# Performance work log

Measured on AMD Instinct MI355X. Metric: run time of the kernel, lower is better.

The kernel has to match this reference:

```python
import jax, jax.numpy as jnp
import numpy as np

NEG_BIG = -9e15
ALPHA = 0.2  # LeakyReLU negative slope
B, N, F_IN, F_OUT = 8, 2048, 128, 128


def setup_inputs() -> dict:
    key = jax.random.key(0)
    k1, k2, k3, k4 = jax.random.split(key, 4)
    inp = jax.random.normal(k1, (B, N, F_IN), dtype=jnp.float32)
    adj = jax.random.randint(k2, (B, N, N), 0, 2, dtype=jnp.int32)
    W = 0.02 * jax.random.normal(k3, (F_OUT, F_IN), dtype=jnp.float32)  # nn.Linear weight [out,in]
    a = 0.02 * jax.random.normal(k4, (1, 2 * F_OUT), dtype=jnp.float32)  # attention vector [1, 2F]
    return {"input": inp, "adj": adj, "W": W, "a": a}


def reference(input, adj, W, a):
    # h = input @ W^T : [B, N, F_OUT]
    h = jnp.einsum("bnf,of->bno", input, W)
    f_out = h.shape[-1]
    # Decompose a . [h_i || h_j] = (h_i . a1) + (h_j . a2) -- same math as the
    # explicit repeat_interleave/repeat/cat, without the O(N^2 * 2F) tensor.
    a1 = a[0, :f_out]
    a2 = a[0, f_out:]
    s1 = h @ a1  # [B, N] score for source node i
    s2 = h @ a2  # [B, N] score for target node j
    e = jax.nn.leaky_relu(s1[:, :, None] + s2[:, None, :], negative_slope=ALPHA)  # [B,N,N]
    masked = jnp.where(adj > 0, e, NEG_BIG)
    attention = jax.nn.softmax(masked, axis=-1)
    # dropout p=0.0 (eval) -> identity
    h_prime = jnp.einsum("bnm,bmo->bno", attention, h)
    return h_prime
```

## Files before the change

kernel.cpp:

```cpp
#include <hip/hip_runtime.h>
#include <stdint.h>


#define B_ 8
#define N_ 2048
#define FD 128
#define ALPHA_ 0.2f
#define TJ 64
#define NCHL 16
#define CHUNK_U4 1024

typedef __attribute__((ext_vector_type(8))) short short8;
typedef __attribute__((ext_vector_type(4))) float f32x4;

#define HCHUNK(o, jc) ((((o) * 16) + ((jc) ^ ((o) & 15))) * 8)
#define HC64(o, jc) ((o) * 8 + ((jc) ^ ((o) & 7)))

__device__ __forceinline__ float bf2f(unsigned short u) {
    union { uint32_t i; float f; } v; v.i = ((uint32_t)u) << 16; return v.f;
}
__device__ __forceinline__ unsigned short f2bf(float f) {
    union { float f; uint32_t i; } v; v.f = f;
    uint32_t x = v.i;
    uint32_t r = (x + 0x7fffu + ((x >> 16) & 1u)) >> 16;
    return (unsigned short)r;
}

__device__ __forceinline__ void gl2lds16(const uint4* g, uint4* l) {
    __builtin_amdgcn_global_load_lds(
        (const __attribute__((address_space(1))) uint32_t*)g,
        (__attribute__((address_space(3))) uint32_t*)l, 16, 0, 0);
}

__global__ __launch_bounds__(256) void gat_h(
    const float* __restrict__ x,
    const float* __restrict__ W,
    const float* __restrict__ a,
    unsigned short* __restrict__ hT,
    float* __restrict__ s1o, float* __restrict__ s2o)
{
    __shared__ __align__(16) unsigned short Wlds[FD * FD];
    __shared__ __align__(16) uint4 xs[64][32];

    const int bid = blockIdx.x;
    const int tid = threadIdx.x;
    const int w = tid >> 6;
    const int lane = tid & 63;
    const int m = lane & 15;
    const int quad = lane >> 4;

#pragma unroll
    for (int it = 0; it < 8; it++) {
        int cid = it * 256 + tid;
        int o = cid >> 4, kc = cid & 15;
        const float* wp = W + (size_t)o * FD + kc * 8;
        float4 w0 = *(const float4*)wp;
        float4 w1 = *(const float4*)(wp + 4);
        uint4 pk;
        pk.x = (uint32_t)f2bf(w0.x) | ((uint32_t)f2bf(w0.y) << 16);
        pk.y = (uint32_t)f2bf(w0.z) | ((uint32_t)f2bf(w0.w) << 16);
        pk.z = (uint32_t)f2bf(w1.x) | ((uint32_t)f2bf(w1.y) << 16);
        pk.w = (uint32_t)f2bf(w1.z) | ((uint32_t)f2bf(w1.w) << 16);
        *(uint4*)&Wlds[HCHUNK(o, kc)] = pk;
    }
#pragma unroll
    for (int it = 0; it < 8; it++) {
        int idx = it * 256 + tid;
        int row = idx >> 5, c = idx & 31;
        uint4 v = *(const uint4*)(x + (size_t)bid * 8192 + (size_t)idx * 4);
        xs[row][c ^ (row & 31)] = v;
    }
    __syncthreads();

    f32x4 acc[8];
#pragma unroll
    for (int ot = 0; ot < 8; ot++) acc[ot] = (f32x4){0.f, 0.f, 0.f, 0.f};

    const int xrow = w * 16 + m;
#pragma unroll
    for (int ks = 0; ks < 4; ks++) {
        const int c0 = ks * 8 + quad * 2;
        union { uint4 u[2]; float f[8]; } xv;
        xv.u[0] = xs[xrow][c0 ^ (xrow & 31)];
        xv.u[1] = xs[xrow][(c0 + 1) ^ (xrow & 31)];
        union { unsigned short us[8]; short8 v; } ahi, alo;
#pragma unroll
        for (int jj = 0; jj < 8; jj++) {
            unsigned short hi = f2bf(xv.f[jj]);
            ahi.us[jj] = hi;
            alo.us[jj] = f2bf(xv.f[jj] - bf2f(hi));
        }
#pragma unroll
        for (int ot = 0; ot < 8; ot++) {
            union { uint4 u; short8 v; } bw;
            bw.u = *(const uint4*)&Wlds[HCHUNK(ot * 16 + m, ks * 4 + quad)];
            acc[ot] = __builtin_amdgcn_mfma_f32_16x16x32_bf16(ahi.v, bw.v, acc[ot], 0, 0, 0);
            acc[ot] = __builtin_amdgcn_mfma_f32_16x16x32_bf16(alo.v, bw.v, acc[ot], 0, 0, 0);
        }
    }

    const int rc0 = bid * 64 + w * 16 + quad * 4;
    const int bb = rc0 >> 11;
    const int jb = rc0 & (N_ - 1);
    const int kc = jb >> 6;
    const int jcl = (jb & 63) >> 3;
    const int off = jb & 7;
    unsigned short* hTb = hT + (size_t)bb * FD * N_ + (size_t)kc * (CHUNK_U4 * 8);
    float s1p[4] = {0.f, 0.f, 0.f, 0.f};
    float s2p[4] = {0.f, 0.f, 0.f, 0.f};
#pragma unroll
    for (int ot = 0; ot < 8; ot++) {
        const int o = ot * 16 + m;
        uint2 pk;
        pk.x = (uint32_t)f2bf(acc[ot][0]) | ((uint32_t)f2bf(acc[ot][1]) << 16);
        pk.y = (uint32_t)f2bf(acc[ot][2]) | ((uint32_t)f2bf(acc[ot][3]) << 16);
        *(uint2*)(hTb + (size_t)HC64(o, jcl) * 8 + off) = pk;
        float a1v = a[o], a2v = a[FD + o];
#pragma unroll
        for (int r = 0; r < 4; r++) {
            s1p[r] += acc[ot][r] * a1v;
            s2p[r] += acc[ot][r] * a2v;
        }
    }
#pragma unroll
    for (int offx = 8; offx >= 1; offx >>= 1) {
#pragma unroll
        for (int r = 0; r < 4; r++) {
            s1p[r] += __shfl_xor(s1p[r], offx);
            s2p[r] += __shfl_xor(s2p[r], offx);
        }
    }
    if (m == 0) {
#pragma unroll
        for (int r = 0; r < 4; r++) {
            s1o[rc0 + r] = s1p[r];
            s2o[rc0 + r] = s2p[r];
        }
    }
}

__global__ __launch_bounds__(256, 2) void gat_attn(
    const int* __restrict__ adj,
    const unsigned short* __restrict__ hT,
    const float* __restrict__ s1,
    const float* __restrict__ s2,
    float* __restrict__ out)
{
    __shared__ __align__(16) uint4 hbuf[2][2][CHUNK_U4];

    const int bid = blockIdx.x;
    const int b = bid & 7;
    const int i0 = (bid >> 3) * 32;
    const int tid = threadIdx.x;
    const int lane = tid & 63;
    const int w = tid >> 6;
    const int jh = w >> 1;
    const int rh = w & 1;
    const int m = lane & 15;
    const int quad = lane >> 4;

    const int irow = i0 + rh * 16 + m;
    const float s1v = s1[b * N_ + irow];
    const int* adjrow = adj + ((size_t)(b * N_ + irow)) * N_ + jh * 1024;
    const uint4* hTc = (const uint4*)(hT + (size_t)b * FD * N_)
                       + (size_t)jh * NCHL * CHUNK_U4;
    const float* s2b = s2 + b * N_ + jh * 1024;

#pragma unroll
    for (int it = 0; it < 8; it++)
        gl2lds16(&hTc[it * 128 + rh * 64 + lane], &hbuf[jh][0][it * 128 + rh * 64]);
    int4 acur[4];
    float4 scur[4];
#pragma unroll
    for (int ks = 0; ks < 2; ks++) {
        acur[2 * ks]     = *(const int4*)(adjrow + ks * 32 + quad * 8);
        acur[2 * ks + 1] = *(const int4*)(adjrow + ks * 32 + quad * 8 + 4);
        scur[2 * ks]     = *(const float4*)(s2b + ks * 32 + quad * 8);
        scur[2 * ks + 1] = *(const float4*)(s2b + ks * 32 + quad * 8 + 4);
    }
    __syncthreads();

    f32x4 acc[8];
#pragma unroll
    for (int ot = 0; ot < 8; ot++) acc[ot] = (f32x4){0.f, 0.f, 0.f, 0.f};
    float rs_loc = 0.f;

    for (int k = 0; k < NCHL; k++) {
        const int buf = k & 1;
        const bool more = (k + 1 < NCHL);
        int4 anext[4];
        float4 snext[4];
        if (more) {
#pragma unroll
            for (int it = 0; it < 8; it++)
                gl2lds16(&hTc[(size_t)(k + 1) * CHUNK_U4 + it * 128 + rh * 64 + lane],
                         &hbuf[jh][buf ^ 1][it * 128 + rh * 64]);
            const int j1 = (k + 1) * TJ;
#pragma unroll
            for (int ks = 0; ks < 2; ks++) {
                anext[2 * ks]     = *(const int4*)(adjrow + j1 + ks * 32 + quad * 8);
                anext[2 * ks + 1] = *(const int4*)(adjrow + j1 + ks * 32 + quad * 8 + 4);
                snext[2 * ks]     = *(const float4*)(s2b + j1 + ks * 32 + quad * 8);
                snext[2 * ks + 1] = *(const float4*)(s2b + j1 + ks * 32 + quad * 8 + 4);
            }
        }

#pragma unroll
        for (int ks = 0; ks < 2; ks++) {
            float4 sa = scur[2 * ks], sb = scur[2 * ks + 1];
            float sarr[8] = {sa.x, sa.y, sa.z, sa.w, sb.x, sb.y, sb.z, sb.w};
            int4 A0 = acur[2 * ks], A1 = acur[2 * ks + 1];
            int aarr[8] = {A0.x, A0.y, A0.z, A0.w, A1.x, A1.y, A1.z, A1.w};
            union { unsigned short us[8]; short8 v; } af;
#pragma unroll
            for (int jj = 0; jj < 8; jj++) {
                float e = s1v + sarr[jj];
                e = (e > 0.f) ? e : (ALPHA_ * e);
                float p = (aarr[jj] > 0) ? __expf(e) : 0.f;
                rs_loc += p;
                af.us[jj] = f2bf(p);
            }
            const int jc = ks * 4 + quad;
#pragma unroll
            for (int ot = 0; ot < 8; ot++) {
                const int o = ot * 16 + m;
                union { uint4 u; short8 v; } bf;
                bf.u = *(const uint4*)&hbuf[jh][buf][HC64(o, jc)];
                acc[ot] = __builtin_amdgcn_mfma_f32_16x16x32_bf16(af.v, bf.v, acc[ot], 0, 0, 0);
            }
        }

        __syncthreads();
        if (more) {
#pragma unroll
            for (int q = 0; q < 4; q++) { acur[q] = anext[q]; scur[q] = snext[q]; }
        }
    }

    float* xch = (float*)&hbuf[0][0][0];
    rs_loc += __shfl_xor(rs_loc, 16);
    rs_loc += __shfl_xor(rs_loc, 32);
    if (jh == 1) {
#pragma unroll
        for (int ot = 0; ot < 8; ot++)
#pragma unroll
            for (int r = 0; r < 4; r++)
                xch[rh * 2048 + (quad * 4 + r) * 128 + ot * 16 + m] = acc[ot][r];
        if (quad == 0) xch[4096 + rh * 16 + m] = rs_loc;
    }
    __syncthreads();
    if (jh == 0) {
        float rinv[4];
#pragma unroll
        for (int r = 0; r < 4; r++) {
            const int p = quad * 4 + r;
            rinv[r] = 1.0f / (__shfl(rs_loc, p) + xch[4096 + rh * 16 + p]);
        }
        float* outp = out + (size_t)(b * N_ + i0 + rh * 16) * FD;
#pragma unroll
        for (int ot = 0; ot < 8; ot++) {
            const int col = ot * 16 + m;
#pragma unroll
            for (int r = 0; r < 4; r++) {
                float v = acc[ot][r] + xch[rh * 2048 + (quad * 4 + r) * 128 + col];
                outp[(size_t)(quad * 4 + r) * FD + col] = v * rinv[r];
            }
        }
    }
}

extern "C" void kernel_launch(void* const* d_in, const int* in_sizes, int n_in,
                              void* d_out, int out_size, void* d_ws, size_t ws_size,
                              hipStream_t stream) {
    const void* xv = d_in[0];
    const void* adjv = d_in[1];
    const void* Wv = d_in[2];
    const void* av = d_in[3];
    for (int i = 0; i < n_in; i++) {
        switch (in_sizes[i]) {
            case 2097152:  xv = d_in[i]; break;
            case 33554432: adjv = d_in[i]; break;
            case 16384:    Wv = d_in[i]; break;
            case 256:      av = d_in[i]; break;
            default: break;
        }
    }
    const float* x = (const float*)xv;
    const int* adj = (const int*)adjv;
    const float* W = (const float*)Wv;
    const float* a = (const float*)av;
    float* out = (float*)d_out;

    char* p = (char*)d_ws;
    unsigned short* hT = (unsigned short*)p;  p += (size_t)B_ * FD * N_ * 2;
    float* s1 = (float*)p;                    p += (size_t)B_ * N_ * 4;
    float* s2 = (float*)p;

    gat_h<<<256, 256, 0, stream>>>(x, W, a, hT, s1, s2);
    gat_attn<<<512, 256, 0, stream>>>(adj, hT, s1, s2, out);
}
```

Before: 218.8 us.

## Pre-pack adjacency into bitmasks in the projection kernel for the attention pass

Extra blocks are added to the first kernel. They read the int32 adjacency matrix and use wave ballots to turn it into 64-bit masks. The attention kernel then reads one uint2 of mask bits per chunk instead of streaming 256 bytes of int32 adjacency per row. This takes the large adjacency loads and their register double-buffering out of the MFMA inner loop. In exchange, the 128 MB adjacency read moves to the pre-kernel and adds a small bitmask write and read.

```diff
diff --git a/kernel.cpp b/kernel.cpp
--- a/kernel.cpp
+++ b/kernel.cpp
@@ -9,6 +9,7 @@
 #define TJ 64
 #define NCHL 16
 #define CHUNK_U4 1024
+#define PACKB 1024
 
 typedef __attribute__((ext_vector_type(8))) short short8;
 typedef __attribute__((ext_vector_type(4))) float f32x4;
@@ -32,12 +33,14 @@
         (__attribute__((address_space(3))) uint32_t*)l, 16, 0, 0);
 }
 
-__global__ __launch_bounds__(256) void gat_h(
+__global__ __launch_bounds__(256) void gat_pre(
     const float* __restrict__ x,
     const float* __restrict__ W,
     const float* __restrict__ a,
+    const int* __restrict__ adj,
     unsigned short* __restrict__ hT,
-    float* __restrict__ s1o, float* __restrict__ s2o)
+    float* __restrict__ s1o, float* __restrict__ s2o,
+    unsigned long long* __restrict__ bits)
 {
     __shared__ __align__(16) unsigned short Wlds[FD * FD];
     __shared__ __align__(16) uint4 xs[64][32];
@@ -46,6 +49,20 @@
     const int tid = threadIdx.x;
     const int w = tid >> 6;
     const int lane = tid & 63;
+
+    if (bid >= 256) {
+        const int wid = (bid - 256) * 4 + w;
+        const int* base = adj + (size_t)wid * 8192;
+        unsigned long long* ob = bits + (size_t)wid * 128;
+#pragma unroll 8
+        for (int it = 0; it < 128; it++) {
+            int v = base[it * 64 + lane];
+            unsigned long long mask = __ballot(v > 0);
+            if (lane == 0) ob[it] = mask;
+        }
+        return;
+    }
+
     const int m = lane & 15;
     const int quad = lane >> 4;
 
@@ -140,7 +157,7 @@
 }
 
 __global__ __launch_bounds__(256, 2) void gat_attn(
-    const int* __restrict__ adj,
+    const unsigned long long* __restrict__ bits,
     const unsigned short* __restrict__ hT,
     const float* __restrict__ s1,
     const float* __restrict__ s2,
@@ -161,7 +178,8 @@
 
     const int irow = i0 + rh * 16 + m;
     const float s1v = s1[b * N_ + irow];
-    const int* adjrow = adj + ((size_t)(b * N_ + irow)) * N_ + jh * 1024;
+    const uint2* bitrow = (const uint2*)(bits + ((size_t)(b * N_ + irow)) * 32
+                                         + jh * NCHL);
     const uint4* hTc = (const uint4*)(hT + (size_t)b * FD * N_)
                        + (size_t)jh * NCHL * CHUNK_U4;
     const float* s2b = s2 + b * N_ + jh * 1024;
@@ -169,12 +187,9 @@
 #pragma unroll
     for (int it = 0; it < 8; it++)
         gl2lds16(&hTc[it * 128 + rh * 64 + lane], &hbuf[jh][0][it * 128 + rh * 64]);
-    int4 acur[4];
     float4 scur[4];
 #pragma unroll
     for (int ks = 0; ks < 2; ks++) {
-        acur[2 * ks]     = *(const int4*)(adjrow + ks * 32 + quad * 8);
-        acur[2 * ks + 1] = *(const int4*)(adjrow + ks * 32 + quad * 8 + 4);
         scur[2 * ks]     = *(const float4*)(s2b + ks * 32 + quad * 8);
         scur[2 * ks + 1] = *(const float4*)(s2b + ks * 32 + quad * 8 + 4);
     }
@@ -188,7 +203,6 @@
     for (int k = 0; k < NCHL; k++) {
         const int buf = k & 1;
         const bool more = (k + 1 < NCHL);
-        int4 anext[4];
         float4 snext[4];
         if (more) {
 #pragma unroll
@@ -198,25 +212,23 @@
             const int j1 = (k + 1) * TJ;
 #pragma unroll
             for (int ks = 0; ks < 2; ks++) {
-                anext[2 * ks]     = *(const int4*)(adjrow + j1 + ks * 32 + quad * 8);
-                anext[2 * ks + 1] = *(const int4*)(adjrow + j1 + ks * 32 + quad * 8 + 4);
                 snext[2 * ks]     = *(const float4*)(s2b + j1 + ks * 32 + quad * 8);
                 snext[2 * ks + 1] = *(const float4*)(s2b + j1 + ks * 32 + quad * 8 + 4);
             }
         }
 
+        const uint2 bm = bitrow[k];
 #pragma unroll
         for (int ks = 0; ks < 2; ks++) {
             float4 sa = scur[2 * ks], sb = scur[2 * ks + 1];
             float sarr[8] = {sa.x, sa.y, sa.z, sa.w, sb.x, sb.y, sb.z, sb.w};
-            int4 A0 = acur[2 * ks], A1 = acur[2 * ks + 1];
-            int aarr[8] = {A0.x, A0.y, A0.z, A0.w, A1.x, A1.y, A1.z, A1.w};
+            const uint32_t byte = ((ks ? bm.y : bm.x) >> (quad * 8)) & 0xffu;
             union { unsigned short us[8]; short8 v; } af;
 #pragma unroll
             for (int jj = 0; jj < 8; jj++) {
                 float e = s1v + sarr[jj];
                 e = (e > 0.f) ? e : (ALPHA_ * e);
-                float p = (aarr[jj] > 0) ? __expf(e) : 0.f;
+                float p = ((byte >> jj) & 1u) ? __expf(e) : 0.f;
                 rs_loc += p;
                 af.us[jj] = f2bf(p);
             }
@@ -233,7 +245,7 @@
         __syncthreads();
         if (more) {
 #pragma unroll
-            for (int q = 0; q < 4; q++) { acur[q] = anext[q]; scur[q] = snext[q]; }
+            for (int q = 0; q < 4; q++) scur[q] = snext[q];
         }
     }
 
@@ -292,10 +304,11 @@
     float* out = (float*)d_out;
 
     char* p = (char*)d_ws;
-    unsigned short* hT = (unsigned short*)p;  p += (size_t)B_ * FD * N_ * 2;
-    float* s1 = (float*)p;                    p += (size_t)B_ * N_ * 4;
-    float* s2 = (float*)p;
-
-    gat_h<<<256, 256, 0, stream>>>(x, W, a, hT, s1, s2);
-    gat_attn<<<512, 256, 0, stream>>>(adj, hT, s1, s2, out);
-}
+    unsigned short* hT = (unsigned short*)p;       p += (size_t)B_ * FD * N_ * 2;
+    float* s1 = (float*)p;                         p += (size_t)B_ * N_ * 4;
+    float* s2 = (float*)p;                         p += (size_t)B_ * N_ * 4;
+    unsigned long long* bits = (unsigned long long*)p;
+
+    gat_pre<<<256 + PACKB, 256, 0, stream>>>(x, W, a, adj, hT, s1, s2, bits);
+    gat_attn<<<512, 256, 0, stream>>>(bits, hT, s1, s2, out);
+}
```

Measured after the change: 325.9 us. 1.49x slower.

## Split gat_h into 512 blocks and load W fragments directly from global

Applied to the files above, without the earlier changes.

The projection kernel now covers 32 rows per block instead of 64 and launches twice as many blocks. The four waves are split two ways over rows and two ways over output columns. The bf16 W tile is no longer staged in shared memory; each wave loads and converts its W fragments straight from global or L2, and the per-row score partials are combined through a small shared buffer. The goal is more parallelism and a shorter prologue in this small kernel, paid for with redundant W conversion and extra global loads.

```diff
diff --git a/kernel.cpp b/kernel.cpp
--- a/kernel.cpp
+++ b/kernel.cpp
@@ -13,7 +13,6 @@
 typedef __attribute__((ext_vector_type(8))) short short8;
 typedef __attribute__((ext_vector_type(4))) float f32x4;
 
-#define HCHUNK(o, jc) ((((o) * 16) + ((jc) ^ ((o) & 15))) * 8)
 #define HC64(o, jc) ((o) * 8 + ((jc) ^ ((o) & 7)))
 
 __device__ __forceinline__ float bf2f(unsigned short u) {
@@ -32,57 +31,45 @@
         (__attribute__((address_space(3))) uint32_t*)l, 16, 0, 0);
 }
 
-__global__ __launch_bounds__(256) void gat_h(
+__global__ __launch_bounds__(256, 4) void gat_h(
     const float* __restrict__ x,
     const float* __restrict__ W,
     const float* __restrict__ a,
     unsigned short* __restrict__ hT,
     float* __restrict__ s1o, float* __restrict__ s2o)
 {
-    __shared__ __align__(16) unsigned short Wlds[FD * FD];
-    __shared__ __align__(16) uint4 xs[64][32];
+    __shared__ __align__(16) uint4 xs[32][32];
+    __shared__ float s1c[2][32], s2c[2][32];
 
     const int bid = blockIdx.x;
     const int tid = threadIdx.x;
     const int w = tid >> 6;
     const int lane = tid & 63;
+    const int oh = w >> 1;
+    const int rh = w & 1;
     const int m = lane & 15;
     const int quad = lane >> 4;
 
 #pragma unroll
-    for (int it = 0; it < 8; it++) {
-        int cid = it * 256 + tid;
-        int o = cid >> 4, kc = cid & 15;
-        const float* wp = W + (size_t)o * FD + kc * 8;
-        float4 w0 = *(const float4*)wp;
-        float4 w1 = *(const float4*)(wp + 4);
-        uint4 pk;
-        pk.x = (uint32_t)f2bf(w0.x) | ((uint32_t)f2bf(w0.y) << 16);
-        pk.y = (uint32_t)f2bf(w0.z) | ((uint32_t)f2bf(w0.w) << 16);
-        pk.z = (uint32_t)f2bf(w1.x) | ((uint32_t)f2bf(w1.y) << 16);
-        pk.w = (uint32_t)f2bf(w1.z) | ((uint32_t)f2bf(w1.w) << 16);
-        *(uint4*)&Wlds[HCHUNK(o, kc)] = pk;
-    }
-#pragma unroll
-    for (int it = 0; it < 8; it++) {
+    for (int it = 0; it < 4; it++) {
         int idx = it * 256 + tid;
         int row = idx >> 5, c = idx & 31;
-        uint4 v = *(const uint4*)(x + (size_t)bid * 8192 + (size_t)idx * 4);
-        xs[row][c ^ (row & 31)] = v;
+        uint4 v = *(const uint4*)(x + (size_t)bid * 4096 + (size_t)idx * 4);
+        xs[row][c ^ row] = v;
     }
     __syncthreads();
 
-    f32x4 acc[8];
-#pragma unroll
-    for (int ot = 0; ot < 8; ot++) acc[ot] = (f32x4){0.f, 0.f, 0.f, 0.f};
-
-    const int xrow = w * 16 + m;
+    f32x4 acc[4];
+#pragma unroll
+    for (int ot = 0; ot < 4; ot++) acc[ot] = (f32x4){0.f, 0.f, 0.f, 0.f};
+
+    const int xrow = rh * 16 + m;
 #pragma unroll
     for (int ks = 0; ks < 4; ks++) {
         const int c0 = ks * 8 + quad * 2;
         union { uint4 u[2]; float f[8]; } xv;
-        xv.u[0] = xs[xrow][c0 ^ (xrow & 31)];
-        xv.u[1] = xs[xrow][(c0 + 1) ^ (xrow & 31)];
+        xv.u[0] = xs[xrow][c0 ^ xrow];
+        xv.u[1] = xs[xrow][(c0 + 1) ^ xrow];
         union { unsigned short us[8]; short8 v; } ahi, alo;
 #pragma unroll
         for (int jj = 0; jj < 8; jj++) {
@@ -91,17 +78,24 @@
             alo.us[jj] = f2bf(xv.f[jj] - bf2f(hi));
         }
 #pragma unroll
-        for (int ot = 0; ot < 8; ot++) {
-            union { uint4 u; short8 v; } bw;
-            bw.u = *(const uint4*)&Wlds[HCHUNK(ot * 16 + m, ks * 4 + quad)];
+        for (int ot = 0; ot < 4; ot++) {
+            const int o = (oh * 4 + ot) * 16 + m;
+            const float* wp = W + (size_t)o * FD + ks * 32 + quad * 8;
+            float4 w0 = *(const float4*)wp;
+            float4 w1 = *(const float4*)(wp + 4);
+            union { unsigned short us[8]; short8 v; } bw;
+            bw.us[0] = f2bf(w0.x); bw.us[1] = f2bf(w0.y);
+            bw.us[2] = f2bf(w0.z); bw.us[3] = f2bf(w0.w);
+            bw.us[4] = f2bf(w1.x); bw.us[5] = f2bf(w1.y);
+            bw.us[6] = f2bf(w1.z); bw.us[7] = f2bf(w1.w);
             acc[ot] = __builtin_amdgcn_mfma_f32_16x16x32_bf16(ahi.v, bw.v, acc[ot], 0, 0, 0);
             acc[ot] = __builtin_amdgcn_mfma_f32_16x16x32_bf16(alo.v, bw.v, acc[ot], 0, 0, 0);
         }
     }
 
-    const int rc0 = bid * 64 + w * 16 + quad * 4;
-    const int bb = rc0 >> 11;
-    const int jb = rc0 & (N_ - 1);
+    const int gr = bid * 32 + rh * 16 + quad * 4;
+    const int bb = gr >> 11;
+    const int jb = gr & (N_ - 1);
     const int kc = jb >> 6;
     const int jcl = (jb & 63) >> 3;
     const int off = jb & 7;
@@ -109,8 +103,8 @@
     float s1p[4] = {0.f, 0.f, 0.f, 0.f};
     float s2p[4] = {0.f, 0.f, 0.f, 0.f};
 #pragma unroll
-    for (int ot = 0; ot < 8; ot++) {
-        const int o = ot * 16 + m;
+    for (int ot = 0; ot < 4; ot++) {
+        const int o = (oh * 4 + ot) * 16 + m;
         uint2 pk;
         pk.x = (uint32_t)f2bf(acc[ot][0]) | ((uint32_t)f2bf(acc[ot][1]) << 16);
         pk.y = (uint32_t)f2bf(acc[ot][2]) | ((uint32_t)f2bf(acc[ot][3]) << 16);
@@ -133,9 +127,14 @@
     if (m == 0) {
 #pragma unroll
         for (int r = 0; r < 4; r++) {
-            s1o[rc0 + r] = s1p[r];
-            s2o[rc0 + r] = s2p[r];
-        }
+            s1c[oh][rh * 16 + quad * 4 + r] = s1p[r];
+            s2c[oh][rh * 16 + quad * 4 + r] = s2p[r];
+        }
+    }
+    __syncthreads();
+    if (tid < 32) {
+        s1o[bid * 32 + tid] = s1c[0][tid] + s1c[1][tid];
+        s2o[bid * 32 + tid] = s2c[0][tid] + s2c[1][tid];
     }
 }
 
@@ -296,6 +295,6 @@
     float* s1 = (float*)p;                    p += (size_t)B_ * N_ * 4;
     float* s2 = (float*)p;
 
-    gat_h<<<256, 256, 0, stream>>>(x, W, a, hT, s1, s2);
+    gat_h<<<512, 256, 0, stream>>>(x, W, a, hT, s1, s2);
     gat_attn<<<512, 256, 0, stream>>>(adj, hT, s1, s2, out);
 }
```

New measurement: 222.7 us. No clear change (+1.8%).
